# Optimization experiments

Hardware: AMD Instinct MI355X
Metric: run time of the kernel (lower is better)

Reference implementation:

```python
import jax, jax.numpy as jnp
import numpy as np

B, N, H = 8, 256, 128
EDGE_IN = 2 * H + 1
NODE_IN = 2 * H


def _glorot(key, shape):
    fan_in, fan_out = shape[0], shape[1]
    lim = 1.0 / np.sqrt(fan_in)
    return jax.random.uniform(key, shape, jnp.float32, -lim, lim)


def setup_inputs() -> dict:
    key = jax.random.key(0)
    ks = jax.random.split(key, 12)
    node_state = jax.random.normal(ks[0], (B, N, H), jnp.float32)
    positions = jax.random.normal(ks[1], (B, N, 3), jnp.float32)
    mask = jnp.ones((B, N), jnp.float32)
    # edge_mlp: Linear(2H+1 -> H), SiLU, Linear(H -> H)  (weights stored [in, out])
    We1 = _glorot(ks[2], (EDGE_IN, H)); be1 = _glorot(ks[3], (1, H))[0]
    We2 = _glorot(ks[4], (H, H));       be2 = _glorot(ks[5], (1, H))[0]
    # node_mlp: Linear(2H -> H), SiLU, Linear(H -> H)
    Wn1 = _glorot(ks[6], (NODE_IN, H)); bn1 = _glorot(ks[7], (1, H))[0]
    Wn2 = _glorot(ks[8], (H, H));       bn2 = _glorot(ks[9], (1, H))[0]
    return {"node_state": node_state, "positions": positions, "mask": mask,
            "We1": We1, "be1": be1, "We2": We2, "be2": be2,
            "Wn1": Wn1, "bn1": bn1, "Wn2": Wn2, "bn2": bn2}


def reference(node_state, positions, mask, We1, be1, We2, be2, Wn1, bn1, Wn2, bn2):
    b, n, h = node_state.shape
    # pairwise distances [B, N, N, 1]; safe-sqrt so grad at i==j is 0 (exact fwd)
    rel = positions[:, :, None, :] - positions[:, None, :, :]
    sq = jnp.sum(rel * rel, axis=-1, keepdims=True)
    dist = jnp.where(sq > 0, jnp.sqrt(jnp.where(sq > 0, sq, 1.0)), 0.0)
    # broadcast-concat node features for all pairs -> [B, N, N, 2H+1]
    node_i = jnp.broadcast_to(node_state[:, :, None, :], (b, n, n, h))
    node_j = jnp.broadcast_to(node_state[:, None, :, :], (b, n, n, h))
    edge_input = jnp.concatenate([node_i, node_j, dist], axis=-1)
    edge_msg = jax.nn.silu(edge_input @ We1 + be1) @ We2 + be2  # [B,N,N,H]
    # pairwise validity mask [B, N, N, 1]
    edge_mask = (mask[:, None, :] * mask[:, :, None])[..., None]
    edge_msg = edge_msg * edge_mask
    # masked mean over j
    denom = jnp.clip(jnp.sum(edge_mask, axis=2), 1.0, None)  # [B,N,1]
    aggregated = jnp.sum(edge_msg, axis=2) / denom           # [B,N,H]
    node_in = jnp.concatenate([node_state, aggregated], axis=-1)
    updated = jax.nn.silu(node_in @ Wn1 + bn1) @ Wn2 + bn2
    return node_state + updated * mask[..., None]
```

## Files before the change

### kernel.cpp

```cpp
#include <hip/hip_runtime.h>
#include <hip/hip_bf16.h>
#include <math.h>

#define B_ 8
#define N_ 256
#define H_ 128
#define NODES_ (B_ * N_)

__device__ __forceinline__ float silu_fast(float x) {
    float e = __expf(-x);
    return x * __builtin_amdgcn_rcpf(1.0f + e);
}

__global__ __launch_bounds__(512) void k1(
    const float* __restrict__ node, const float* __restrict__ We1,
    const float* __restrict__ be1, const float* __restrict__ Wn1,
    const float* __restrict__ bn1, const float* __restrict__ mask,
    float* __restrict__ P, float* __restrict__ Q, float* __restrict__ pre)
{
    __shared__ float act[4][128];
    __shared__ float pls[16][4][128];
    const int t = threadIdx.x;
    const int g = blockIdx.x >> 9;
    const int node0 = (blockIdx.x & 511) * 4;

    if (t < 128) {
        int r = t >> 5, col = (t & 31) * 4;
        *(float4*)(&act[r][col]) = *(const float4*)(node + (size_t)(node0 + r) * H_ + col);
    }
    const float* W = (g == 0) ? We1 : (g == 1) ? (We1 + 128 * H_) : Wn1;
    const int kseg = t >> 5;
    const int c0   = (t & 31) * 4;
    __syncthreads();

    float4 w[8];
    const float* Wb = W + (size_t)(kseg * 8) * H_ + c0;
    #pragma unroll
    for (int u = 0; u < 8; ++u) w[u] = *(const float4*)(Wb + u * H_);

    #pragma unroll
    for (int n = 0; n < 4; ++n) {
        float4 a = {0.f, 0.f, 0.f, 0.f};
        #pragma unroll
        for (int u = 0; u < 8; ++u) {
            float v = act[n][kseg * 8 + u];
            a.x = fmaf(v, w[u].x, a.x);
            a.y = fmaf(v, w[u].y, a.y);
            a.z = fmaf(v, w[u].z, a.z);
            a.w = fmaf(v, w[u].w, a.w);
        }
        *(float4*)(&pls[kseg][n][c0]) = a;
    }
    __syncthreads();

    {
        const int n = t >> 7;
        const int c = t & 127;
        float s = 0.f;
        #pragma unroll
        for (int seg = 0; seg < 16; ++seg) s += pls[seg][n][c];
        float* op;
        if (g == 0)      { op = P;   s += be1[c]; }
        else if (g == 1) { op = Q;   s += (mask[node0 + n] - 1.0f) * 1e30f; }
        else             { op = pre; s += bn1[c]; }
        op[(size_t)(node0 + n) * H_ + c] = s;
    }
}

__global__ __launch_bounds__(512) void k2bc(
    const float* __restrict__ P, const float* __restrict__ Q,
    const float* __restrict__ We1, const float* __restrict__ positions,
    const float* __restrict__ mask, const float* __restrict__ pre,
    const float* __restrict__ node,
    const float* __restrict__ We2, const float* __restrict__ be2,
    const float* __restrict__ Wn1, const float* __restrict__ Wn2,
    const float* __restrict__ bn2, float* __restrict__ out)
{
    __shared__ float arena[8192];
    __shared__ float dls[256][4];
    __shared__ float Sls[4][128];
    __shared__ float Tls[4][128];
    __shared__ float cs;
    const int t  = threadIdx.x;
    const int b  = blockIdx.x >> 6;
    const int i0 = (blockIdx.x & 63) * 4;

    {
        const int t2 = t & 255;
        const int half = t >> 8;
        const int il = t2 & 3;
        const int jb = t2 >> 2;
        const float* pb = positions + b * N_ * 3;
        const float pix = pb[(i0 + il) * 3 + 0];
        const float piy = pb[(i0 + il) * 3 + 1];
        const float piz = pb[(i0 + il) * 3 + 2];
        #pragma unroll
        for (int s = 0; s < 2; ++s) {
            int j = jb + 64 * (half * 2 + s);
            float dx = pix - pb[j * 3 + 0];
            float dy = piy - pb[j * 3 + 1];
            float dz = piz - pb[j * 3 + 2];
            float sq = dx * dx + dy * dy + dz * dz;
            dls[j][il] = (sq > 0.f) ? sqrtf(sq) : 0.f;
        }
    }
    if (t < 64) {
        float mv = mask[b * N_ + t] + mask[b * N_ + 64 + t]
                 + mask[b * N_ + 128 + t] + mask[b * N_ + 192 + t];
        #pragma unroll
        for (int off = 32; off >= 1; off >>= 1) mv += __shfl_down(mv, off);
        if (t == 0) cs = mv;
    }

    const int i = t >> 7;
    const int c = t & 127;
    const float wd   = We1[256 * H_ + c];
    const float base = P[(size_t)(b * N_ + i0 + i) * H_ + c];
    const float4* __restrict__ Qg = (const float4*)(Q + (size_t)(b * N_) * H_);

    float4 r0 = Qg[0 * 512 + t];
    float4 r1 = Qg[1 * 512 + t];
    float4 r2 = Qg[2 * 512 + t];
    float4 r3 = Qg[3 * 512 + t];

    float acc = 0.f;
    for (int ch = 0; ch < 4; ++ch) {
        __syncthreads();
        ((float4*)arena)[0 * 512 + t] = r0;
        ((float4*)arena)[1 * 512 + t] = r1;
        ((float4*)arena)[2 * 512 + t] = r2;
        ((float4*)arena)[3 * 512 + t] = r3;
        if (ch < 3) {
            r0 = Qg[(ch + 1) * 2048 + 0 * 512 + t];
            r1 = Qg[(ch + 1) * 2048 + 1 * 512 + t];
            r2 = Qg[(ch + 1) * 2048 + 2 * 512 + t];
            r3 = Qg[(ch + 1) * 2048 + 3 * 512 + t];
        }
        __syncthreads();
        const int j0 = ch * 64;
        #pragma unroll 8
        for (int jj = 0; jj < 64; ++jj) {
            float q = arena[jj * 128 + c];
            float d = dls[j0 + jj][i];
            float x = fmaf(d, wd, base + q);
            float e = __expf(-x);
            float r = __builtin_amdgcn_rcpf(1.0f + e);
            acc = fmaf(x, r, acc);
        }
    }

    const float inv_cnt = __builtin_amdgcn_rcpf(fmaxf(cs, 1.0f));
    const float mi = mask[b * N_ + i0 + i];
    Sls[i][c] = (mi * inv_cnt) * acc;
    __syncthreads();

    float (*pls)[4][128] = (float (*)[4][128])arena;
    const int kseg = t >> 5;
    const int c0   = (t & 31) * 4;

    {
        const float* Wb = We2 + (size_t)(kseg * 8) * H_ + c0;
        float4 w[8];
        #pragma unroll
        for (int u = 0; u < 8; ++u) w[u] = *(const float4*)(Wb + u * H_);
        #pragma unroll
        for (int n = 0; n < 4; ++n) {
            float4 a = {0.f, 0.f, 0.f, 0.f};
            #pragma unroll
            for (int u = 0; u < 8; ++u) {
                float v = Sls[n][kseg * 8 + u];
                a.x = fmaf(v, w[u].x, a.x); a.y = fmaf(v, w[u].y, a.y);
                a.z = fmaf(v, w[u].z, a.z); a.w = fmaf(v, w[u].w, a.w);
            }
            *(float4*)(&pls[kseg][n][c0]) = a;
        }
    }
    __syncthreads();
    {
        float s = 0.f;
        #pragma unroll
        for (int seg = 0; seg < 16; ++seg) s += pls[seg][i][c];
        Tls[i][c] = fmaf(mi, be2[c], s);
    }
    __syncthreads();

    {
        const float* Wb = Wn1 + (size_t)(128 + kseg * 8) * H_ + c0;
        float4 w[8];
        #pragma unroll
        for (int u = 0; u < 8; ++u) w[u] = *(const float4*)(Wb + u * H_);
        #pragma unroll
        for (int n = 0; n < 4; ++n) {
            float4 a = {0.f, 0.f, 0.f, 0.f};
            #pragma unroll
            for (int u = 0; u < 8; ++u) {
                float v = Tls[n][kseg * 8 + u];
                a.x = fmaf(v, w[u].x, a.x); a.y = fmaf(v, w[u].y, a.y);
                a.z = fmaf(v, w[u].z, a.z); a.w = fmaf(v, w[u].w, a.w);
            }
            *(float4*)(&pls[kseg][n][c0]) = a;
        }
    }
    __syncthreads();
    {
        float s = 0.f;
        #pragma unroll
        for (int seg = 0; seg < 16; ++seg) s += pls[seg][i][c];
        float h = silu_fast(pre[(size_t)(b * N_ + i0 + i) * H_ + c] + s);
        Sls[i][c] = h;
    }
    __syncthreads();

    {
        const float* Wb = Wn2 + (size_t)(kseg * 8) * H_ + c0;
        float4 w[8];
        #pragma unroll
        for (int u = 0; u < 8; ++u) w[u] = *(const float4*)(Wb + u * H_);
        #pragma unroll
        for (int n = 0; n < 4; ++n) {
            float4 a = {0.f, 0.f, 0.f, 0.f};
            #pragma unroll
            for (int u = 0; u < 8; ++u) {
                float v = Sls[n][kseg * 8 + u];
                a.x = fmaf(v, w[u].x, a.x); a.y = fmaf(v, w[u].y, a.y);
                a.z = fmaf(v, w[u].z, a.z); a.w = fmaf(v, w[u].w, a.w);
            }
            *(float4*)(&pls[kseg][n][c0]) = a;
        }
    }
    __syncthreads();
    {
        float s = 0.f;
        #pragma unroll
        for (int seg = 0; seg < 16; ++seg) s += pls[seg][i][c];
        const size_t idx = (size_t)(b * N_ + i0 + i) * H_ + c;
        out[idx] = node[idx] + mi * (s + bn2[c]);
    }
}

extern "C" void kernel_launch(void* const* d_in, const int* in_sizes, int n_in,
                              void* d_out, int out_size, void* d_ws, size_t ws_size,
                              hipStream_t stream)
{
    const float* node      = (const float*)d_in[0];
    const float* positions = (const float*)d_in[1];
    const float* mask      = (const float*)d_in[2];
    const float* We1       = (const float*)d_in[3];
    const float* be1       = (const float*)d_in[4];
    const float* We2       = (const float*)d_in[5];
    const float* be2       = (const float*)d_in[6];
    const float* Wn1       = (const float*)d_in[7];
    const float* bn1       = (const float*)d_in[8];
    const float* Wn2       = (const float*)d_in[9];
    const float* bn2       = (const float*)d_in[10];
    float* out = (float*)d_out;

    const size_t SZ = (size_t)NODES_ * H_;
    float* P   = (float*)d_ws;
    float* Q   = P + SZ;
    float* pre = Q + SZ;

    k1  <<<1536, 512, 0, stream>>>(node, We1, be1, Wn1, bn1, mask, P, Q, pre);
    k2bc<<<512,  512, 0, stream>>>(P, Q, We1, positions, mask, pre, node,
                                   We2, be2, Wn1, Wn2, bn2, out);
}
```

Baseline: 103.3 us.

## Halve k2bc block size and compute two edge rows per thread

```diff
diff --git a/kernel.cpp b/kernel.cpp
--- a/kernel.cpp
+++ b/kernel.cpp
@@ -18,8 +18,8 @@
     const float* __restrict__ bn1, const float* __restrict__ mask,
     float* __restrict__ P, float* __restrict__ Q, float* __restrict__ pre)
 {
-    __shared__ float act[4][128];
-    __shared__ float pls[16][4][128];
+    __shared__ __align__(16) float act[4][128];
+    __shared__ __align__(16) float pls[16][4][128];
     const int t = threadIdx.x;
     const int g = blockIdx.x >> 9;
     const int node0 = (blockIdx.x & 511) * 4;
@@ -67,7 +67,7 @@
     }
 }
 
-__global__ __launch_bounds__(512) void k2bc(
+__global__ __launch_bounds__(256) void k2bc(
     const float* __restrict__ P, const float* __restrict__ Q,
     const float* __restrict__ We1, const float* __restrict__ positions,
     const float* __restrict__ mask, const float* __restrict__ pre,
@@ -76,8 +76,8 @@
     const float* __restrict__ Wn1, const float* __restrict__ Wn2,
     const float* __restrict__ bn2, float* __restrict__ out)
 {
-    __shared__ float arena[8192];
-    __shared__ float dls[256][4];
+    __shared__ __align__(16) float arena[8192];
+    __shared__ __align__(16) float dt[4][260];
     __shared__ float Sls[4][128];
     __shared__ float Tls[4][128];
     __shared__ float cs;
@@ -86,22 +86,17 @@
     const int i0 = (blockIdx.x & 63) * 4;
 
     {
-        const int t2 = t & 255;
-        const int half = t >> 8;
-        const int il = t2 & 3;
-        const int jb = t2 >> 2;
         const float* pb = positions + b * N_ * 3;
-        const float pix = pb[(i0 + il) * 3 + 0];
-        const float piy = pb[(i0 + il) * 3 + 1];
-        const float piz = pb[(i0 + il) * 3 + 2];
-        #pragma unroll
-        for (int s = 0; s < 2; ++s) {
-            int j = jb + 64 * (half * 2 + s);
-            float dx = pix - pb[j * 3 + 0];
-            float dy = piy - pb[j * 3 + 1];
-            float dz = piz - pb[j * 3 + 2];
+        const float pjx = pb[t * 3 + 0];
+        const float pjy = pb[t * 3 + 1];
+        const float pjz = pb[t * 3 + 2];
+        #pragma unroll
+        for (int il = 0; il < 4; ++il) {
+            float dx = pb[(i0 + il) * 3 + 0] - pjx;
+            float dy = pb[(i0 + il) * 3 + 1] - pjy;
+            float dz = pb[(i0 + il) * 3 + 2] - pjz;
             float sq = dx * dx + dy * dy + dz * dz;
-            dls[j][il] = (sq > 0.f) ? sqrtf(sq) : 0.f;
+            dt[il][t] = (sq > 0.f) ? sqrtf(sq) : 0.f;
         }
     }
     if (t < 64) {
@@ -112,46 +107,55 @@
         if (t == 0) cs = mv;
     }
 
-    const int i = t >> 7;
+    const int g = t >> 7;
     const int c = t & 127;
-    const float wd   = We1[256 * H_ + c];
-    const float base = P[(size_t)(b * N_ + i0 + i) * H_ + c];
+    const int iA = i0 + 2 * g;
+    const float wd    = We1[256 * H_ + c];
+    const float baseA = P[(size_t)(b * N_ + iA)     * H_ + c];
+    const float baseB = P[(size_t)(b * N_ + iA + 1) * H_ + c];
     const float4* __restrict__ Qg = (const float4*)(Q + (size_t)(b * N_) * H_);
 
-    float4 r0 = Qg[0 * 512 + t];
-    float4 r1 = Qg[1 * 512 + t];
-    float4 r2 = Qg[2 * 512 + t];
-    float4 r3 = Qg[3 * 512 + t];
-
-    float acc = 0.f;
+    float4 r[8];
+    #pragma unroll
+    for (int u = 0; u < 8; ++u) r[u] = Qg[u * 256 + t];
+
+    float accA = 0.f, accB = 0.f;
     for (int ch = 0; ch < 4; ++ch) {
         __syncthreads();
-        ((float4*)arena)[0 * 512 + t] = r0;
-        ((float4*)arena)[1 * 512 + t] = r1;
-        ((float4*)arena)[2 * 512 + t] = r2;
-        ((float4*)arena)[3 * 512 + t] = r3;
+        #pragma unroll
+        for (int u = 0; u < 8; ++u) ((float4*)arena)[u * 256 + t] = r[u];
         if (ch < 3) {
-            r0 = Qg[(ch + 1) * 2048 + 0 * 512 + t];
-            r1 = Qg[(ch + 1) * 2048 + 1 * 512 + t];
-            r2 = Qg[(ch + 1) * 2048 + 2 * 512 + t];
-            r3 = Qg[(ch + 1) * 2048 + 3 * 512 + t];
+            #pragma unroll
+            for (int u = 0; u < 8; ++u) r[u] = Qg[(ch + 1) * 2048 + u * 256 + t];
         }
         __syncthreads();
         const int j0 = ch * 64;
-        #pragma unroll 8
-        for (int jj = 0; jj < 64; ++jj) {
-            float q = arena[jj * 128 + c];
-            float d = dls[j0 + jj][i];
-            float x = fmaf(d, wd, base + q);
-            float e = __expf(-x);
-            float r = __builtin_amdgcn_rcpf(1.0f + e);
-            acc = fmaf(x, r, acc);
+        #pragma unroll 4
+        for (int jw = 0; jw < 64; jw += 4) {
+            float4 dA = *(const float4*)(&dt[2 * g][j0 + jw]);
+            float4 dB = *(const float4*)(&dt[2 * g + 1][j0 + jw]);
+            #pragma unroll
+            for (int u = 0; u < 4; ++u) {
+                float q  = arena[(jw + u) * 128 + c];
+                float du0 = (u == 0) ? dA.x : (u == 1) ? dA.y : (u == 2) ? dA.z : dA.w;
+                float du1 = (u == 0) ? dB.x : (u == 1) ? dB.y : (u == 2) ? dB.z : dB.w;
+                float xA = fmaf(du0, wd, baseA + q);
+                float xB = fmaf(du1, wd, baseB + q);
+                float eA = __expf(-xA);
+                float eB = __expf(-xB);
+                float rA = __builtin_amdgcn_rcpf(1.0f + eA);
+                float rB = __builtin_amdgcn_rcpf(1.0f + eB);
+                accA = fmaf(xA, rA, accA);
+                accB = fmaf(xB, rB, accB);
+            }
         }
     }
 
     const float inv_cnt = __builtin_amdgcn_rcpf(fmaxf(cs, 1.0f));
-    const float mi = mask[b * N_ + i0 + i];
-    Sls[i][c] = (mi * inv_cnt) * acc;
+    const float miA = mask[b * N_ + iA];
+    const float miB = mask[b * N_ + iA + 1];
+    Sls[2 * g][c]     = (miA * inv_cnt) * accA;
+    Sls[2 * g + 1][c] = (miB * inv_cnt) * accB;
     __syncthreads();
 
     float (*pls)[4][128] = (float (*)[4][128])arena;
@@ -159,82 +163,107 @@
     const int c0   = (t & 31) * 4;
 
     {
-        const float* Wb = We2 + (size_t)(kseg * 8) * H_ + c0;
-        float4 w[8];
-        #pragma unroll
-        for (int u = 0; u < 8; ++u) w[u] = *(const float4*)(Wb + u * H_);
-        #pragma unroll
-        for (int n = 0; n < 4; ++n) {
-            float4 a = {0.f, 0.f, 0.f, 0.f};
-            #pragma unroll
-            for (int u = 0; u < 8; ++u) {
-                float v = Sls[n][kseg * 8 + u];
-                a.x = fmaf(v, w[u].x, a.x); a.y = fmaf(v, w[u].y, a.y);
-                a.z = fmaf(v, w[u].z, a.z); a.w = fmaf(v, w[u].w, a.w);
-            }
-            *(float4*)(&pls[kseg][n][c0]) = a;
-        }
-    }
-    __syncthreads();
-    {
-        float s = 0.f;
-        #pragma unroll
-        for (int seg = 0; seg < 16; ++seg) s += pls[seg][i][c];
-        Tls[i][c] = fmaf(mi, be2[c], s);
-    }
-    __syncthreads();
-
-    {
-        const float* Wb = Wn1 + (size_t)(128 + kseg * 8) * H_ + c0;
-        float4 w[8];
-        #pragma unroll
-        for (int u = 0; u < 8; ++u) w[u] = *(const float4*)(Wb + u * H_);
-        #pragma unroll
-        for (int n = 0; n < 4; ++n) {
-            float4 a = {0.f, 0.f, 0.f, 0.f};
-            #pragma unroll
-            for (int u = 0; u < 8; ++u) {
-                float v = Tls[n][kseg * 8 + u];
-                a.x = fmaf(v, w[u].x, a.x); a.y = fmaf(v, w[u].y, a.y);
-                a.z = fmaf(v, w[u].z, a.z); a.w = fmaf(v, w[u].w, a.w);
-            }
-            *(float4*)(&pls[kseg][n][c0]) = a;
-        }
-    }
-    __syncthreads();
-    {
-        float s = 0.f;
-        #pragma unroll
-        for (int seg = 0; seg < 16; ++seg) s += pls[seg][i][c];
-        float h = silu_fast(pre[(size_t)(b * N_ + i0 + i) * H_ + c] + s);
-        Sls[i][c] = h;
-    }
-    __syncthreads();
-
-    {
-        const float* Wb = Wn2 + (size_t)(kseg * 8) * H_ + c0;
-        float4 w[8];
-        #pragma unroll
-        for (int u = 0; u < 8; ++u) w[u] = *(const float4*)(Wb + u * H_);
-        #pragma unroll
-        for (int n = 0; n < 4; ++n) {
-            float4 a = {0.f, 0.f, 0.f, 0.f};
-            #pragma unroll
-            for (int u = 0; u < 8; ++u) {
-                float v = Sls[n][kseg * 8 + u];
-                a.x = fmaf(v, w[u].x, a.x); a.y = fmaf(v, w[u].y, a.y);
-                a.z = fmaf(v, w[u].z, a.z); a.w = fmaf(v, w[u].w, a.w);
-            }
-            *(float4*)(&pls[kseg][n][c0]) = a;
-        }
-    }
-    __syncthreads();
-    {
-        float s = 0.f;
-        #pragma unroll
-        for (int seg = 0; seg < 16; ++seg) s += pls[seg][i][c];
-        const size_t idx = (size_t)(b * N_ + i0 + i) * H_ + c;
-        out[idx] = node[idx] + mi * (s + bn2[c]);
+        float4 a[4] = {{0,0,0,0},{0,0,0,0},{0,0,0,0},{0,0,0,0}};
+        #pragma unroll
+        for (int h = 0; h < 2; ++h) {
+            const float* Wb = We2 + (size_t)(kseg * 16 + h * 8) * H_ + c0;
+            float4 w[8];
+            #pragma unroll
+            for (int u = 0; u < 8; ++u) w[u] = *(const float4*)(Wb + u * H_);
+            #pragma unroll
+            for (int n = 0; n < 4; ++n) {
+                #pragma unroll
+                for (int u = 0; u < 8; ++u) {
+                    float v = Sls[n][kseg * 16 + h * 8 + u];
+                    a[n].x = fmaf(v, w[u].x, a[n].x); a[n].y = fmaf(v, w[u].y, a[n].y);
+                    a[n].z = fmaf(v, w[u].z, a[n].z); a[n].w = fmaf(v, w[u].w, a[n].w);
+                }
+            }
+        }
+        #pragma unroll
+        for (int n = 0; n < 4; ++n) *(float4*)(&pls[kseg][n][c0]) = a[n];
+    }
+    __syncthreads();
+    {
+        #pragma unroll
+        for (int p = 0; p < 2; ++p) {
+            const int n = 2 * g + p;
+            float s = 0.f;
+            #pragma unroll
+            for (int seg = 0; seg < 8; ++seg) s += pls[seg][n][c];
+            const float mi = mask[b * N_ + i0 + n];
+            Tls[n][c] = fmaf(mi, be2[c], s);
+        }
+    }
+    __syncthreads();
+
+    {
+        float4 a[4] = {{0,0,0,0},{0,0,0,0},{0,0,0,0},{0,0,0,0}};
+        #pragma unroll
+        for (int h = 0; h < 2; ++h) {
+            const float* Wb = Wn1 + (size_t)(128 + kseg * 16 + h * 8) * H_ + c0;
+            float4 w[8];
+            #pragma unroll
+            for (int u = 0; u < 8; ++u) w[u] = *(const float4*)(Wb + u * H_);
+            #pragma unroll
+            for (int n = 0; n < 4; ++n) {
+                #pragma unroll
+                for (int u = 0; u < 8; ++u) {
+                    float v = Tls[n][kseg * 16 + h * 8 + u];
+                    a[n].x = fmaf(v, w[u].x, a[n].x); a[n].y = fmaf(v, w[u].y, a[n].y);
+                    a[n].z = fmaf(v, w[u].z, a[n].z); a[n].w = fmaf(v, w[u].w, a[n].w);
+                }
+            }
+        }
+        #pragma unroll
+        for (int n = 0; n < 4; ++n) *(float4*)(&pls[kseg][n][c0]) = a[n];
+    }
+    __syncthreads();
+    {
+        #pragma unroll
+        for (int p = 0; p < 2; ++p) {
+            const int n = 2 * g + p;
+            float s = 0.f;
+            #pragma unroll
+            for (int seg = 0; seg < 8; ++seg) s += pls[seg][n][c];
+            Sls[n][c] = silu_fast(pre[(size_t)(b * N_ + i0 + n) * H_ + c] + s);
+        }
+    }
+    __syncthreads();
+
+    {
+        float4 a[4] = {{0,0,0,0},{0,0,0,0},{0,0,0,0},{0,0,0,0}};
+        #pragma unroll
+        for (int h = 0; h < 2; ++h) {
+            const float* Wb = Wn2 + (size_t)(kseg * 16 + h * 8) * H_ + c0;
+            float4 w[8];
+            #pragma unroll
+            for (int u = 0; u < 8; ++u) w[u] = *(const float4*)(Wb + u * H_);
+            #pragma unroll
+            for (int n = 0; n < 4; ++n) {
+                #pragma unroll
+                for (int u = 0; u < 8; ++u) {
+                    float v = Sls[n][kseg * 16 + h * 8 + u];
+                    a[n].x = fmaf(v, w[u].x, a[n].x); a[n].y = fmaf(v, w[u].y, a[n].y);
+                    a[n].z = fmaf(v, w[u].z, a[n].z); a[n].w = fmaf(v, w[u].w, a[n].w);
+                }
+            }
+        }
+        #pragma unroll
+        for (int n = 0; n < 4; ++n) *(float4*)(&pls[kseg][n][c0]) = a[n];
+    }
+    __syncthreads();
+    {
+        #pragma unroll
+        for (int p = 0; p < 2; ++p) {
+            const int n = 2 * g + p;
+            float s = 0.f;
+            #pragma unroll
+            for (int seg = 0; seg < 8; ++seg) s += pls[seg][n][c];
+            const float mi = mask[b * N_ + i0 + n];
+            const size_t idx = (size_t)(b * N_ + i0 + n) * H_ + c;
+            out[idx] = node[idx] + mi * (s + bn2[c]);
+        }
     }
 }
 
@@ -261,6 +290,6 @@
     float* pre = Q + SZ;
 
     k1  <<<1536, 512, 0, stream>>>(node, We1, be1, Wn1, bn1, mask, P, Q, pre);
-    k2bc<<<512,  512, 0, stream>>>(P, Q, We1, positions, mask, pre, node,
+    k2bc<<<512,  256, 0, stream>>>(P, Q, We1, positions, mask, pre, node,
                                    We2, be2, Wn1, Wn2, bn2, out);
 }
```

After: 116.5 us. 12.8% more time.
